# Kernel optimization log

Measured on AMD Instinct MI355X. Metric: run time of the kernel, lower is better.

The kernel has to match this reference:

```python
import jax, jax.numpy as jnp
import numpy as np

N = 1536       # number of agents in the group
T = 20         # track length (only last step used)
H = 64         # hidden_size
E = 16         # embadding_size
M = 128        # PNMLP_hidden_size


def setup_inputs() -> dict:
    key = jax.random.key(0)
    ks = jax.random.split(key, 8)
    s = lambda fan_in: 1.0 / np.sqrt(fan_in)
    return {
        "hidden_state": jax.random.normal(ks[0], (N, H), dtype=jnp.float32),
        "group_track": jax.random.normal(ks[1], (N, T, 2), dtype=jnp.float32),
        "We": jax.random.uniform(ks[2], (2, E), jnp.float32, -s(2), s(2)),
        "be": jax.random.uniform(ks[3], (E,), jnp.float32, -s(2), s(2)),
        "W1": jax.random.uniform(ks[4], (E + H, M), jnp.float32, -s(E + H), s(E + H)),
        "b1": jax.random.uniform(ks[5], (M,), jnp.float32, -s(E + H), s(E + H)),
        "W2": jax.random.uniform(ks[6], (M, H), jnp.float32, -s(M), s(M)),
        "b2": jax.random.uniform(ks[7], (H,), jnp.float32, -s(M), s(M)),
    }


def reference(hidden_state, group_track, We, be, W1, b1, W2, b2):
    # end positions of every track: [N, 2]
    end = group_track[:, -1, :]
    # rel[i, j] = end[j] - end[i]  (neighbor j relative to center i): [N, N, 2]
    rel = end[None, :, :] - end[:, None, :]
    # linear embedding of relative end positions: [N, N, E]
    emb = rel @ We + be
    # concat hidden state (same for all centers) with embedding: [N, N, E+H]
    h = jnp.broadcast_to(hidden_state[None, :, :], (rel.shape[0], rel.shape[1], hidden_state.shape[1]))
    x = jnp.concatenate((h, emb), axis=-1)
    # MLP [E+H -> M -> H] with ReLU after each linear (batch_norm=False)
    x = jax.nn.relu(x @ W1 + b1)
    x = jax.nn.relu(x @ W2 + b2)
    # max-pool over neighbors j for each center i: [N, H]
    return jnp.max(x, axis=1)
```

## Files before the change

kernel.cpp:

```cpp
#include <hip/hip_runtime.h>


#define NN 1536
#define HH 64
#define EE 16
#define MM 128
#define TT 20

#define JSPLIT 2
#define NTILE (96 / JSPLIT)

typedef _Float16 half8 __attribute__((ext_vector_type(8)));
typedef float f32x4 __attribute__((ext_vector_type(4)));

__global__ __launch_bounds__(128) void precompute_kernel(
    const float* __restrict__ hidden, const float* __restrict__ gt,
    const float* __restrict__ We, const float* __restrict__ be,
    const float* __restrict__ W1, const float* __restrict__ b1,
    const float* __restrict__ W2,
    _Float16* __restrict__ Qf, _Float16* __restrict__ P,
    _Float16* __restrict__ W2f, float* __restrict__ out)
{
  const int j = blockIdx.x;
  const int m = threadIdx.x;
  const float* hrow = hidden + j * HH;
  float a0 = 0.f, a1 = 0.f;
  #pragma unroll 8
  for (int h = 0; h < HH; h += 2) {
    a0 = fmaf(hrow[h],     W1[h * MM + m],       a0);
    a1 = fmaf(hrow[h + 1], W1[(h + 1) * MM + m], a1);
  }
  const float a = a0 + a1;
  float ve0 = 0.f, ve1 = 0.f, cm = b1[m];
  #pragma unroll
  for (int e = 0; e < EE; ++e) {
    float w1e = W1[(HH + e) * MM + m];
    ve0 = fmaf(We[e], w1e, ve0);
    ve1 = fmaf(We[EE + e], w1e, ve1);
    cm  = fmaf(be[e], w1e, cm);
  }
  const float e0 = gt[j * (2 * TT) + 2 * (TT - 1)];
  const float e1 = gt[j * (2 * TT) + 2 * (TT - 1) + 1];
  const float p = fmaf(e0, ve0, e1 * ve1);
  P[j * MM + m] = (_Float16)p;

  const int jt = j >> 4;
  const int ks = m >> 5;
  const int ln = ((m >> 3) & 3) * 16 + (j & 15);
  const int jj = m & 7;
  Qf[(((jt * 4) + ks) * 64 + ln) * 8 + jj] = (_Float16)(a + p + cm);

  if (m < HH) out[j * HH + m] = 0.f;

  if (j < 8) {
    const int u = j * 128 + m;
    const int ct = u >> 8;
    const int ksx = (u >> 6) & 3;
    const int l = u & 63;
    half8 w;
    #pragma unroll
    for (int t = 0; t < 8; ++t)
      w[t] = (_Float16)W2[(ksx * 32 + (l >> 4) * 8 + t) * HH + ct * 16 + (l & 15)];
    *(half8*)(W2f + (size_t)u * 8) = w;
  }
}

__global__ __launch_bounds__(64, 3) void pairmlp_max_kernel(
    const _Float16* __restrict__ Qf, const _Float16* __restrict__ P,
    const _Float16* __restrict__ W2f, const float* __restrict__ b2,
    float* __restrict__ out)
{
  const int lane = threadIdx.x;
  const int quad = lane >> 4;
  const int lcol = lane & 15;
  const int i  = blockIdx.x % NN;
  const int js = blockIdx.x / NN;

  half8 bfrag[4][4];
  {
    const half8* wf = (const half8*)W2f + lane;
    #pragma unroll
    for (int ct = 0; ct < 4; ++ct)
      #pragma unroll
      for (int ks = 0; ks < 4; ++ks)
        bfrag[ct][ks] = wf[(ct * 4 + ks) * 64];
  }

  half8 pv[4];
  #pragma unroll
  for (int ks = 0; ks < 4; ++ks)
    pv[ks] = *(const half8*)(P + i * MM + ks * 32 + quad * 8);

  float b2v[4];
  #pragma unroll
  for (int ct = 0; ct < 4; ++ct) b2v[ct] = b2[ct * 16 + lcol];

  float rmax[4];
  #pragma unroll
  for (int ct = 0; ct < 4; ++ct) rmax[ct] = -3.0e38f;

  const int jt0 = js * NTILE;
  const half8* qbase = (const half8*)Qf + (size_t)jt0 * 256 + lane;

  half8 qc[4], qn[4];
  #pragma unroll
  for (int ks = 0; ks < 4; ++ks) qc[ks] = qbase[ks * 64];

  const half8 hz = 0;

  for (int t = 0; t < NTILE; ++t) {
    const int tn = (t + 1 < NTILE) ? (t + 1) : 0;
    #pragma unroll
    for (int ks = 0; ks < 4; ++ks)
      qn[ks] = qbase[(size_t)tn * 256 + ks * 64];

    f32x4 acc[4];
    {
      half8 s = qc[0] - pv[0];
      s = __builtin_elementwise_max(s, hz);
      #pragma unroll
      for (int ct = 0; ct < 4; ++ct)
        acc[ct] = __builtin_amdgcn_mfma_f32_16x16x32_f16(s, bfrag[ct][0], f32x4{0.f, 0.f, 0.f, 0.f}, 0, 0, 0);
    }
    #pragma unroll
    for (int ks = 1; ks < 4; ++ks) {
      half8 s = qc[ks] - pv[ks];
      s = __builtin_elementwise_max(s, hz);
      #pragma unroll
      for (int ct = 0; ct < 4; ++ct)
        acc[ct] = __builtin_amdgcn_mfma_f32_16x16x32_f16(s, bfrag[ct][ks], acc[ct], 0, 0, 0);
    }

    #pragma unroll
    for (int ct = 0; ct < 4; ++ct) {
      const float m01 = fmaxf(acc[ct][0], acc[ct][1]);
      const float m23 = fmaxf(acc[ct][2], acc[ct][3]);
      rmax[ct] = fmaxf(rmax[ct], fmaxf(m01, m23));
    }

    #pragma unroll
    for (int ks = 0; ks < 4; ++ks) qc[ks] = qn[ks];
  }

  #pragma unroll
  for (int ct = 0; ct < 4; ++ct) {
    float v = rmax[ct];
    v = fmaxf(v, __shfl_xor(v, 16, 64));
    v = fmaxf(v, __shfl_xor(v, 32, 64));
    v = fmaxf(v + b2v[ct], 0.f);
    if (quad == 0)
      atomicMax((unsigned*)(out + i * HH + ct * 16 + lcol), __float_as_uint(v));
  }
}

extern "C" void kernel_launch(void* const* d_in, const int* in_sizes, int n_in,
                              void* d_out, int out_size, void* d_ws, size_t ws_size,
                              hipStream_t stream) {
  const float* hidden = (const float*)d_in[0];
  const float* gt     = (const float*)d_in[1];
  const float* We     = (const float*)d_in[2];
  const float* be     = (const float*)d_in[3];
  const float* W1     = (const float*)d_in[4];
  const float* b1     = (const float*)d_in[5];
  const float* W2     = (const float*)d_in[6];
  const float* b2     = (const float*)d_in[7];
  float* out = (float*)d_out;

  _Float16* Qf  = (_Float16*)d_ws;
  _Float16* Ph  = Qf + NN * MM;
  _Float16* W2f = Ph + NN * MM;

  precompute_kernel<<<NN, 128, 0, stream>>>(hidden, gt, We, be, W1, b1, W2, Qf, Ph, W2f, out);
  pairmlp_max_kernel<<<NN * JSPLIT, 64, 0, stream>>>(Qf, Ph, W2f, b2, out);
}
```

Baseline: 119.4 us.

## Process three centers per wave to reuse loaded neighbor tiles across MFMAs

Each wave now handles three center rows i, so every loaded Q tile of 16 neighbors is reused across three sets of MFMAs. This cuts global/L2 traffic per MFMA and amortizes load latency. The j dimension is split four ways instead of two to keep enough blocks, and the loop is unrolled by two with ping-pong prefetch buffers and s_setprio around the MFMA bursts. Occupancy hint drops to 2 because register pressure grows with the extra accumulators and P vectors.

```diff
diff --git a/kernel.cpp b/kernel.cpp
--- a/kernel.cpp
+++ b/kernel.cpp
@@ -7,7 +7,9 @@
 #define MM 128
 #define TT 20
 
-#define JSPLIT 2
+#define NI 3
+#define NIGRP (NN / NI)
+#define JSPLIT 4
 #define NTILE (96 / JSPLIT)
 
 typedef _Float16 half8 __attribute__((ext_vector_type(8)));
@@ -65,7 +67,7 @@
   }
 }
 
-__global__ __launch_bounds__(64, 3) void pairmlp_max_kernel(
+__global__ __launch_bounds__(64, 2) void pairmlp_max_kernel(
     const _Float16* __restrict__ Qf, const _Float16* __restrict__ P,
     const _Float16* __restrict__ W2f, const float* __restrict__ b2,
     float* __restrict__ out)
@@ -73,8 +75,9 @@
   const int lane = threadIdx.x;
   const int quad = lane >> 4;
   const int lcol = lane & 15;
-  const int i  = blockIdx.x % NN;
-  const int js = blockIdx.x / NN;
+  const int ig = blockIdx.x % NIGRP;
+  const int js = blockIdx.x / NIGRP;
+  const int i0 = ig * NI;
 
   half8 bfrag[4][4];
   {
@@ -86,71 +89,88 @@
         bfrag[ct][ks] = wf[(ct * 4 + ks) * 64];
   }
 
-  half8 pv[4];
+  half8 pv[NI][4];
   #pragma unroll
-  for (int ks = 0; ks < 4; ++ks)
-    pv[ks] = *(const half8*)(P + i * MM + ks * 32 + quad * 8);
+  for (int ii = 0; ii < NI; ++ii) {
+    const _Float16* prow = P + (i0 + ii) * MM + quad * 8;
+    #pragma unroll
+    for (int ks = 0; ks < 4; ++ks)
+      pv[ii][ks] = *(const half8*)(prow + ks * 32);
+  }
 
   float b2v[4];
   #pragma unroll
   for (int ct = 0; ct < 4; ++ct) b2v[ct] = b2[ct * 16 + lcol];
 
-  float rmax[4];
+  float rmax[NI][4];
   #pragma unroll
-  for (int ct = 0; ct < 4; ++ct) rmax[ct] = -3.0e38f;
+  for (int ii = 0; ii < NI; ++ii)
+    #pragma unroll
+    for (int ct = 0; ct < 4; ++ct) rmax[ii][ct] = -3.0e38f;
 
   const int jt0 = js * NTILE;
   const half8* qbase = (const half8*)Qf + (size_t)jt0 * 256 + lane;
+
+  const half8 hz = 0;
+
+  auto compute_tile = [&](const half8* qt) {
+    f32x4 acc[NI][4];
+    #pragma unroll
+    for (int ks = 0; ks < 4; ++ks) {
+      __builtin_amdgcn_s_setprio(1);
+      #pragma unroll
+      for (int ii = 0; ii < NI; ++ii) {
+        half8 s = qt[ks] - pv[ii][ks];
+        s = __builtin_elementwise_max(s, hz);
+        #pragma unroll
+        for (int ct = 0; ct < 4; ++ct) {
+          if (ks == 0)
+            acc[ii][ct] = __builtin_amdgcn_mfma_f32_16x16x32_f16(
+                s, bfrag[ct][0], f32x4{0.f, 0.f, 0.f, 0.f}, 0, 0, 0);
+          else
+            acc[ii][ct] = __builtin_amdgcn_mfma_f32_16x16x32_f16(
+                s, bfrag[ct][ks], acc[ii][ct], 0, 0, 0);
+        }
+      }
+      __builtin_amdgcn_s_setprio(0);
+    }
+    #pragma unroll
+    for (int ii = 0; ii < NI; ++ii)
+      #pragma unroll
+      for (int ct = 0; ct < 4; ++ct) {
+        const float t3 = fmaxf(fmaxf(acc[ii][ct][0], acc[ii][ct][1]), acc[ii][ct][2]);
+        rmax[ii][ct] = fmaxf(fmaxf(t3, acc[ii][ct][3]), rmax[ii][ct]);
+      }
+  };
 
   half8 qc[4], qn[4];
   #pragma unroll
   for (int ks = 0; ks < 4; ++ks) qc[ks] = qbase[ks * 64];
 
-  const half8 hz = 0;
-
-  for (int t = 0; t < NTILE; ++t) {
-    const int tn = (t + 1 < NTILE) ? (t + 1) : 0;
+  for (int t = 0; t < NTILE; t += 2) {
     #pragma unroll
     for (int ks = 0; ks < 4; ++ks)
-      qn[ks] = qbase[(size_t)tn * 256 + ks * 64];
+      qn[ks] = qbase[(size_t)(t + 1) * 256 + ks * 64];
+    compute_tile(qc);
 
-    f32x4 acc[4];
-    {
-      half8 s = qc[0] - pv[0];
-      s = __builtin_elementwise_max(s, hz);
-      #pragma unroll
-      for (int ct = 0; ct < 4; ++ct)
-        acc[ct] = __builtin_amdgcn_mfma_f32_16x16x32_f16(s, bfrag[ct][0], f32x4{0.f, 0.f, 0.f, 0.f}, 0, 0, 0);
-    }
+    const int t2 = (t + 2 < NTILE) ? (t + 2) : 0;
     #pragma unroll
-    for (int ks = 1; ks < 4; ++ks) {
-      half8 s = qc[ks] - pv[ks];
-      s = __builtin_elementwise_max(s, hz);
-      #pragma unroll
-      for (int ct = 0; ct < 4; ++ct)
-        acc[ct] = __builtin_amdgcn_mfma_f32_16x16x32_f16(s, bfrag[ct][ks], acc[ct], 0, 0, 0);
-    }
-
-    #pragma unroll
-    for (int ct = 0; ct < 4; ++ct) {
-      const float m01 = fmaxf(acc[ct][0], acc[ct][1]);
-      const float m23 = fmaxf(acc[ct][2], acc[ct][3]);
-      rmax[ct] = fmaxf(rmax[ct], fmaxf(m01, m23));
-    }
-
-    #pragma unroll
-    for (int ks = 0; ks < 4; ++ks) qc[ks] = qn[ks];
+    for (int ks = 0; ks < 4; ++ks)
+      qc[ks] = qbase[(size_t)t2 * 256 + ks * 64];
+    compute_tile(qn);
   }
 
   #pragma unroll
-  for (int ct = 0; ct < 4; ++ct) {
-    float v = rmax[ct];
-    v = fmaxf(v, __shfl_xor(v, 16, 64));
-    v = fmaxf(v, __shfl_xor(v, 32, 64));
-    v = fmaxf(v + b2v[ct], 0.f);
-    if (quad == 0)
-      atomicMax((unsigned*)(out + i * HH + ct * 16 + lcol), __float_as_uint(v));
-  }
+  for (int ii = 0; ii < NI; ++ii)
+    #pragma unroll
+    for (int ct = 0; ct < 4; ++ct) {
+      float v = rmax[ii][ct];
+      v = fmaxf(v, __shfl_xor(v, 16, 64));
+      v = fmaxf(v, __shfl_xor(v, 32, 64));
+      v = fmaxf(v + b2v[ct], 0.f);
+      if (quad == 0)
+        atomicMax((unsigned*)(out + (i0 + ii) * HH + ct * 16 + lcol), __float_as_uint(v));
+    }
 }
 
 extern "C" void kernel_launch(void* const* d_in, const int* in_sizes, int n_in,
@@ -171,5 +191,5 @@
   _Float16* W2f = Ph + NN * MM;
 
   precompute_kernel<<<NN, 128, 0, stream>>>(hidden, gt, We, be, W1, b1, W2, Qf, Ph, W2f, out);
-  pairmlp_max_kernel<<<NN * JSPLIT, 64, 0, stream>>>(Qf, Ph, W2f, b2, out);
+  pairmlp_max_kernel<<<NIGRP * JSPLIT, 64, 0, stream>>>(Qf, Ph, W2f, b2, out);
 }
```

Result: faster. 103.1 us (-13.7%).

## Switch pair MLP to 32x32x16 MFMA tiles with split-run prefetch and setprio

Applied to the files above, without the earlier changes.

Changes the second-layer matmul from 16x16x32 MFMA to 32x32x16 MFMA. This requires re-laying out Qf and the W2 fragments into 32-row tiles with 8 k-steps. The tile loop is split into two halves whose starting order alternates by block parity, is unrolled by two with double-buffered register prefetch, and wraps MFMA bursts in s_setprio. The goal is fewer MFMA issues per tile, lower instruction overhead and spread-out memory access, at the cost of higher register pressure (launch bounds lowered to 2 waves per SIMD).

```diff
diff --git a/kernel.cpp b/kernel.cpp
--- a/kernel.cpp
+++ b/kernel.cpp
@@ -8,10 +8,12 @@
 #define TT 20
 
 #define JSPLIT 2
-#define NTILE (96 / JSPLIT)
+#define NT32 (NN / 32)
+#define NTILE (NT32 / JSPLIT)
+#define HTILE (NTILE / 2)
 
 typedef _Float16 half8 __attribute__((ext_vector_type(8)));
-typedef float f32x4 __attribute__((ext_vector_type(4)));
+typedef float f32x16 __attribute__((ext_vector_type(16)));
 
 __global__ __launch_bounds__(128) void precompute_kernel(
     const float* __restrict__ hidden, const float* __restrict__ gt,
@@ -44,112 +46,130 @@
   const float p = fmaf(e0, ve0, e1 * ve1);
   P[j * MM + m] = (_Float16)p;
 
-  const int jt = j >> 4;
-  const int ks = m >> 5;
-  const int ln = ((m >> 3) & 3) * 16 + (j & 15);
+  const int ks = m >> 4;
+  const int hi = (m >> 3) & 1;
   const int jj = m & 7;
-  Qf[(((jt * 4) + ks) * 64 + ln) * 8 + jj] = (_Float16)(a + p + cm);
+  const int l  = hi * 32 + (j & 31);
+  Qf[((((j >> 5) * 8) + ks) * 64 + l) * 8 + jj] = (_Float16)(a + p + cm);
 
   if (m < HH) out[j * HH + m] = 0.f;
 
   if (j < 8) {
     const int u = j * 128 + m;
-    const int ct = u >> 8;
-    const int ksx = (u >> 6) & 3;
-    const int l = u & 63;
+    const int ct = u >> 9;
+    const int ksx = (u >> 6) & 7;
+    const int lx = u & 63;
     half8 w;
     #pragma unroll
     for (int t = 0; t < 8; ++t)
-      w[t] = (_Float16)W2[(ksx * 32 + (l >> 4) * 8 + t) * HH + ct * 16 + (l & 15)];
+      w[t] = (_Float16)W2[(ksx * 16 + (lx >> 5) * 8 + t) * HH + ct * 32 + (lx & 31)];
     *(half8*)(W2f + (size_t)u * 8) = w;
   }
 }
 
-__global__ __launch_bounds__(64, 3) void pairmlp_max_kernel(
+__global__ __launch_bounds__(64, 2) void pairmlp_max_kernel(
     const _Float16* __restrict__ Qf, const _Float16* __restrict__ P,
     const _Float16* __restrict__ W2f, const float* __restrict__ b2,
     float* __restrict__ out)
 {
   const int lane = threadIdx.x;
-  const int quad = lane >> 4;
-  const int lcol = lane & 15;
+  const int lc32 = lane & 31;
+  const int hi   = lane >> 5;
   const int i  = blockIdx.x % NN;
   const int js = blockIdx.x / NN;
+  const int par = blockIdx.x & 1;
 
-  half8 bfrag[4][4];
+  half8 bfrag[2][8];
   {
     const half8* wf = (const half8*)W2f + lane;
     #pragma unroll
-    for (int ct = 0; ct < 4; ++ct)
+    for (int ct = 0; ct < 2; ++ct)
       #pragma unroll
-      for (int ks = 0; ks < 4; ++ks)
-        bfrag[ct][ks] = wf[(ct * 4 + ks) * 64];
+      for (int ks = 0; ks < 8; ++ks)
+        bfrag[ct][ks] = wf[(ct * 8 + ks) * 64];
   }
 
-  half8 pv[4];
+  half8 pv[8];
+  {
+    const _Float16* prow = P + i * MM + hi * 8;
+    #pragma unroll
+    for (int ks = 0; ks < 8; ++ks)
+      pv[ks] = *(const half8*)(prow + ks * 16);
+  }
+
+  float b2v[2];
   #pragma unroll
-  for (int ks = 0; ks < 4; ++ks)
-    pv[ks] = *(const half8*)(P + i * MM + ks * 32 + quad * 8);
+  for (int ct = 0; ct < 2; ++ct) b2v[ct] = b2[ct * 32 + lc32];
 
-  float b2v[4];
-  #pragma unroll
-  for (int ct = 0; ct < 4; ++ct) b2v[ct] = b2[ct * 16 + lcol];
+  float rmax[2] = {-3.0e38f, -3.0e38f};
 
-  float rmax[4];
-  #pragma unroll
-  for (int ct = 0; ct < 4; ++ct) rmax[ct] = -3.0e38f;
-
-  const int jt0 = js * NTILE;
-  const half8* qbase = (const half8*)Qf + (size_t)jt0 * 256 + lane;
-
-  half8 qc[4], qn[4];
-  #pragma unroll
-  for (int ks = 0; ks < 4; ++ks) qc[ks] = qbase[ks * 64];
+  const char* qbytes = (const char*)Qf + (size_t)(js * NTILE) * 8192 + lane * 16;
 
   const half8 hz = 0;
+  const f32x16 fz = {0.f,0.f,0.f,0.f,0.f,0.f,0.f,0.f,0.f,0.f,0.f,0.f,0.f,0.f,0.f,0.f};
 
-  for (int t = 0; t < NTILE; ++t) {
-    const int tn = (t + 1 < NTILE) ? (t + 1) : 0;
-    #pragma unroll
-    for (int ks = 0; ks < 4; ++ks)
-      qn[ks] = qbase[(size_t)tn * 256 + ks * 64];
-
-    f32x4 acc[4];
+  auto compute_tile = [&](const half8* qt) {
+    f32x16 acc0, acc1;
+    __builtin_amdgcn_s_setprio(1);
     {
-      half8 s = qc[0] - pv[0];
+      half8 s = qt[0] - pv[0];
       s = __builtin_elementwise_max(s, hz);
-      #pragma unroll
-      for (int ct = 0; ct < 4; ++ct)
-        acc[ct] = __builtin_amdgcn_mfma_f32_16x16x32_f16(s, bfrag[ct][0], f32x4{0.f, 0.f, 0.f, 0.f}, 0, 0, 0);
+      acc0 = __builtin_amdgcn_mfma_f32_32x32x16_f16(s, bfrag[0][0], fz, 0, 0, 0);
+      acc1 = __builtin_amdgcn_mfma_f32_32x32x16_f16(s, bfrag[1][0], fz, 0, 0, 0);
     }
     #pragma unroll
-    for (int ks = 1; ks < 4; ++ks) {
-      half8 s = qc[ks] - pv[ks];
+    for (int ks = 1; ks < 8; ++ks) {
+      half8 s = qt[ks] - pv[ks];
       s = __builtin_elementwise_max(s, hz);
-      #pragma unroll
-      for (int ct = 0; ct < 4; ++ct)
-        acc[ct] = __builtin_amdgcn_mfma_f32_16x16x32_f16(s, bfrag[ct][ks], acc[ct], 0, 0, 0);
+      acc0 = __builtin_amdgcn_mfma_f32_32x32x16_f16(s, bfrag[0][ks], acc0, 0, 0, 0);
+      acc1 = __builtin_amdgcn_mfma_f32_32x32x16_f16(s, bfrag[1][ks], acc1, 0, 0, 0);
     }
+    __builtin_amdgcn_s_setprio(0);
+    float m0a = fmaxf(fmaxf(acc0[0], acc0[1]), fmaxf(acc0[2], acc0[3]));
+    float m0b = fmaxf(fmaxf(acc0[4], acc0[5]), fmaxf(acc0[6], acc0[7]));
+    float m0c = fmaxf(fmaxf(acc0[8], acc0[9]), fmaxf(acc0[10], acc0[11]));
+    float m0d = fmaxf(fmaxf(acc0[12], acc0[13]), fmaxf(acc0[14], acc0[15]));
+    rmax[0] = fmaxf(rmax[0], fmaxf(fmaxf(m0a, m0b), fmaxf(m0c, m0d)));
+    float m1a = fmaxf(fmaxf(acc1[0], acc1[1]), fmaxf(acc1[2], acc1[3]));
+    float m1b = fmaxf(fmaxf(acc1[4], acc1[5]), fmaxf(acc1[6], acc1[7]));
+    float m1c = fmaxf(fmaxf(acc1[8], acc1[9]), fmaxf(acc1[10], acc1[11]));
+    float m1d = fmaxf(fmaxf(acc1[12], acc1[13]), fmaxf(acc1[14], acc1[15]));
+    rmax[1] = fmaxf(rmax[1], fmaxf(fmaxf(m1a, m1b), fmaxf(m1c, m1d)));
+  };
+
+  half8 qc[8], qn[8];
+
+  for (int h = 0; h < 2; ++h) {
+    const char* runb = qbytes + (((h ^ par) != 0) ? HTILE * 8192 : 0);
+    const char* qp = runb;
 
     #pragma unroll
-    for (int ct = 0; ct < 4; ++ct) {
-      const float m01 = fmaxf(acc[ct][0], acc[ct][1]);
-      const float m23 = fmaxf(acc[ct][2], acc[ct][3]);
-      rmax[ct] = fmaxf(rmax[ct], fmaxf(m01, m23));
+    for (int ks = 0; ks < 8; ++ks)
+      qc[ks] = *(const half8*)(qp + ks * 1024);
+
+    for (int t = 0; t < HTILE; t += 2) {
+      #pragma unroll
+      for (int ks = 0; ks < 8; ++ks)
+        qn[ks] = *(const half8*)(qp + 8192 + ks * 1024);
+      compute_tile(qc);
+
+      const char* q2 = (t + 2 < HTILE) ? (qp + 16384) : runb;
+      #pragma unroll
+      for (int ks = 0; ks < 8; ++ks)
+        qc[ks] = *(const half8*)(q2 + ks * 1024);
+      compute_tile(qn);
+
+      qp += 16384;
     }
-
-    #pragma unroll
-    for (int ks = 0; ks < 4; ++ks) qc[ks] = qn[ks];
   }
 
   #pragma unroll
-  for (int ct = 0; ct < 4; ++ct) {
+  for (int ct = 0; ct < 2; ++ct) {
     float v = rmax[ct];
-    v = fmaxf(v, __shfl_xor(v, 16, 64));
     v = fmaxf(v, __shfl_xor(v, 32, 64));
     v = fmaxf(v + b2v[ct], 0.f);
-    if (quad == 0)
-      atomicMax((unsigned*)(out + i * HH + ct * 16 + lcol), __float_as_uint(v));
+    if (hi == 0)
+      atomicMax((unsigned*)(out + i * HH + ct * 32 + lc32), __float_as_uint(v));
   }
 }
 
```

Measured after the change: 110.6 us. 7.4% less time.

## Pack eight waves per block, split neighbors four ways, unroll tile loop by two

Applied to the files above, without the earlier changes.

The pair-MLP kernel now runs eight independent waves per 512-thread block instead of one wave per block, and splits the neighbor range into four chunks instead of two. The main loop is unrolled by two with double-buffered Q loads, and s_setprio raises wave priority around the MFMA section. The aim is better CU occupancy and latency hiding, plus less per-block launch overhead. In exchange, twice as many atomicMax writes hit the output, and register pressure under the new launch bounds may limit occupancy.

```diff
diff --git a/kernel.cpp b/kernel.cpp
--- a/kernel.cpp
+++ b/kernel.cpp
@@ -7,8 +7,9 @@
 #define MM 128
 #define TT 20
 
-#define JSPLIT 2
+#define JSPLIT 4
 #define NTILE (96 / JSPLIT)
+#define BW 8
 
 typedef _Float16 half8 __attribute__((ext_vector_type(8)));
 typedef float f32x4 __attribute__((ext_vector_type(4)));
@@ -65,16 +66,18 @@
   }
 }
 
-__global__ __launch_bounds__(64, 3) void pairmlp_max_kernel(
+__global__ __launch_bounds__(512, 4) void pairmlp_max_kernel(
     const _Float16* __restrict__ Qf, const _Float16* __restrict__ P,
     const _Float16* __restrict__ W2f, const float* __restrict__ b2,
     float* __restrict__ out)
 {
-  const int lane = threadIdx.x;
+  const int lane = threadIdx.x & 63;
+  const int wid  = threadIdx.x >> 6;
   const int quad = lane >> 4;
   const int lcol = lane & 15;
-  const int i  = blockIdx.x % NN;
-  const int js = blockIdx.x / NN;
+  const int gid = blockIdx.x * BW + wid;
+  const int i  = gid % NN;
+  const int js = gid / NN;
 
   half8 bfrag[4][4];
   {
@@ -87,59 +90,68 @@
   }
 
   half8 pv[4];
-  #pragma unroll
-  for (int ks = 0; ks < 4; ++ks)
-    pv[ks] = *(const half8*)(P + i * MM + ks * 32 + quad * 8);
-
-  float b2v[4];
-  #pragma unroll
-  for (int ct = 0; ct < 4; ++ct) b2v[ct] = b2[ct * 16 + lcol];
+  {
+    const _Float16* prow = P + i * MM + quad * 8;
+    #pragma unroll
+    for (int ks = 0; ks < 4; ++ks)
+      pv[ks] = *(const half8*)(prow + ks * 32);
+  }
 
   float rmax[4];
   #pragma unroll
   for (int ct = 0; ct < 4; ++ct) rmax[ct] = -3.0e38f;
 
-  const int jt0 = js * NTILE;
-  const half8* qbase = (const half8*)Qf + (size_t)jt0 * 256 + lane;
-
-  half8 qc[4], qn[4];
-  #pragma unroll
-  for (int ks = 0; ks < 4; ++ks) qc[ks] = qbase[ks * 64];
+  const char* qp = (const char*)Qf + (size_t)(js * NTILE) * 4096 + lane * 16;
 
   const half8 hz = 0;
+  const f32x4 fz = {0.f, 0.f, 0.f, 0.f};
 
-  for (int t = 0; t < NTILE; ++t) {
-    const int tn = (t + 1 < NTILE) ? (t + 1) : 0;
-    #pragma unroll
-    for (int ks = 0; ks < 4; ++ks)
-      qn[ks] = qbase[(size_t)tn * 256 + ks * 64];
-
+  auto compute_tile = [&](const half8* qt) {
     f32x4 acc[4];
+    __builtin_amdgcn_s_setprio(1);
     {
-      half8 s = qc[0] - pv[0];
+      half8 s = qt[0] - pv[0];
       s = __builtin_elementwise_max(s, hz);
       #pragma unroll
       for (int ct = 0; ct < 4; ++ct)
-        acc[ct] = __builtin_amdgcn_mfma_f32_16x16x32_f16(s, bfrag[ct][0], f32x4{0.f, 0.f, 0.f, 0.f}, 0, 0, 0);
+        acc[ct] = __builtin_amdgcn_mfma_f32_16x16x32_f16(s, bfrag[ct][0], fz, 0, 0, 0);
     }
     #pragma unroll
     for (int ks = 1; ks < 4; ++ks) {
-      half8 s = qc[ks] - pv[ks];
+      half8 s = qt[ks] - pv[ks];
       s = __builtin_elementwise_max(s, hz);
       #pragma unroll
       for (int ct = 0; ct < 4; ++ct)
         acc[ct] = __builtin_amdgcn_mfma_f32_16x16x32_f16(s, bfrag[ct][ks], acc[ct], 0, 0, 0);
     }
-
+    __builtin_amdgcn_s_setprio(0);
     #pragma unroll
     for (int ct = 0; ct < 4; ++ct) {
-      const float m01 = fmaxf(acc[ct][0], acc[ct][1]);
-      const float m23 = fmaxf(acc[ct][2], acc[ct][3]);
-      rmax[ct] = fmaxf(rmax[ct], fmaxf(m01, m23));
+      const float t3 = fmaxf(fmaxf(acc[ct][0], acc[ct][1]), acc[ct][2]);
+      rmax[ct] = fmaxf(fmaxf(t3, acc[ct][3]), rmax[ct]);
     }
+  };
 
+  half8 qc[4], qn[4];
+
+  #pragma unroll
+  for (int ks = 0; ks < 4; ++ks)
+    qc[ks] = *(const half8*)(qp + ks * 1024);
+
+  for (int t = 0; t < NTILE; t += 2) {
     #pragma unroll
-    for (int ks = 0; ks < 4; ++ks) qc[ks] = qn[ks];
+    for (int ks = 0; ks < 4; ++ks)
+      qn[ks] = *(const half8*)(qp + 4096 + ks * 1024);
+    compute_tile(qc);
+
+    const char* q2 = (t + 2 < NTILE) ? (qp + 8192)
+                                     : ((const char*)Qf + (size_t)(js * NTILE) * 4096 + lane * 16);
+    #pragma unroll
+    for (int ks = 0; ks < 4; ++ks)
+      qc[ks] = *(const half8*)(q2 + ks * 1024);
+    compute_tile(qn);
+
+    qp += 8192;
   }
 
   #pragma unroll
@@ -147,7 +159,7 @@
     float v = rmax[ct];
     v = fmaxf(v, __shfl_xor(v, 16, 64));
     v = fmaxf(v, __shfl_xor(v, 32, 64));
-    v = fmaxf(v + b2v[ct], 0.f);
+    v = fmaxf(v + b2[ct * 16 + lcol], 0.f);
     if (quad == 0)
       atomicMax((unsigned*)(out + i * HH + ct * 16 + lcol), __float_as_uint(v));
   }
@@ -171,5 +183,5 @@
   _Float16* W2f = Ph + NN * MM;
 
   precompute_kernel<<<NN, 128, 0, stream>>>(hidden, gt, We, be, W1, b1, W2, Qf, Ph, W2f, out);
-  pairmlp_max_kernel<<<NN * JSPLIT, 64, 0, stream>>>(Qf, Ph, W2f, b2, out);
+  pairmlp_max_kernel<<<(NN * JSPLIT) / BW, 512, 0, stream>>>(Qf, Ph, W2f, b2, out);
 }
```

Measured after the change: 187.2 us. +56.8%, slower.
